# Optimization experiments

Measured on AMD Instinct MI355X. Metric: run time of the kernel, lower is better.

The kernel has to match this reference:

```python
import jax, jax.numpy as jnp
import numpy as np

B, C, H, W = 2, 256, 64, 64
NH, HD, K = 4, 64, 16  # num_head, head_channel, n_clusters
N = H * W
SCALE = HD ** 0.5


def _lin(x, Wm, b):
    return x @ Wm + b


def _mlp(x, W1, b1, W2, b2):
    h = _lin(x, W1, b1)
    h = jnp.where(h > 0, h, 0.01 * h)  # LeakyReLU(0.01)
    return _lin(h, W2, b2)  # dropout p=0.0 -> identity


def setup_inputs() -> dict:
    key = jax.random.key(0)
    ks = jax.random.split(key, 20)
    s = 1.0 / np.sqrt(C)
    s2 = 1.0 / np.sqrt(2 * C)
    inp = {
        "q_img": jax.random.normal(ks[0], (B, C, H, W), jnp.float32),
        "k_img_map": jax.random.normal(ks[1], (B, C, H, W), jnp.float32),
        "v_img_map": jax.random.normal(ks[2], (B, C, H, W), jnp.float32),
        "labels": jax.random.randint(ks[3], (B, H, W), 0, K),
        "pixel_coefficients": jax.random.uniform(ks[4], (B, N, N), jnp.float32),
        "Wq": jax.random.uniform(ks[5], (C, C), jnp.float32, -s, s),
        "bq": jnp.zeros((C,), jnp.float32),
        "Wk": jax.random.uniform(ks[6], (C, C), jnp.float32, -s, s),
        "bk": jnp.zeros((C,), jnp.float32),
        "Wv": jax.random.uniform(ks[7], (C, C), jnp.float32, -s, s),
        "bv": jnp.zeros((C,), jnp.float32),
        "W11": jax.random.uniform(ks[8], (C, 2 * C), jnp.float32, -s, s),
        "b11": jnp.zeros((2 * C,), jnp.float32),
        "W12": jax.random.uniform(ks[9], (2 * C, C), jnp.float32, -s2, s2),
        "b12": jnp.zeros((C,), jnp.float32),
        "W21": jax.random.uniform(ks[10], (C, 2 * C), jnp.float32, -s, s),
        "b21": jnp.zeros((2 * C,), jnp.float32),
        "W22": jax.random.uniform(ks[11], (2 * C, C), jnp.float32, -s2, s2),
        "b22": jnp.zeros((C,), jnp.float32),
    }
    return inp


def reference(q_img, k_img_map, v_img_map, labels, pixel_coefficients,
              Wq, bq, Wk, bk, Wv, bv, W11, b11, W12, b12, W21, b21, W22, b22):
    # [B,C,H,W] -> [B,N,C]
    q = _lin(q_img.transpose(0, 2, 3, 1).reshape(B, N, C), Wq, bq)
    k = _lin(k_img_map.transpose(0, 2, 3, 1).reshape(B, N, C), Wk, bk)
    v = _lin(v_img_map.transpose(0, 2, 3, 1).reshape(B, N, C), Wv, bv)

    lab = labels.reshape(B, N)
    onehot = (lab[:, :, None] == jnp.arange(K)[None, None, :]).astype(jnp.float32)  # [B,N,K]
    num_k = jnp.einsum('bnk,bnc->bkc', onehot, k)
    den_k = onehot.sum(axis=1)[:, :, None] + 1e-6
    centers_k = num_k / den_k  # [B,K,C]

    qm = q.reshape(B, N, NH, HD).transpose(0, 2, 1, 3)  # [B,h,N,d]
    km = k.reshape(B, N, NH, HD).transpose(0, 2, 1, 3)
    vm = v.reshape(B, N, NH, HD).transpose(0, 2, 1, 3)
    cm = centers_k.reshape(B, K, NH, HD).transpose(0, 2, 1, 3)  # [B,h,K,d]

    attn_intra = jnp.einsum('bhnd,bhmd->bhnm', qm, km)          # [B,h,N,N]
    attn_centers = jnp.einsum('bhnd,bhkd->bhnk', qm, cm)        # [B,h,N,K]

    same = (lab[:, :, None] == lab[:, None, :])[:, None]        # [B,1,N,N]
    idx = jnp.broadcast_to(lab[:, None, None, :], (B, NH, N, N))
    attn_inter = jnp.take_along_axis(attn_centers, idx, axis=-1) * pixel_coefficients[:, None]

    scores = jnp.where(same, attn_intra, attn_inter) / SCALE
    attn = jax.nn.softmax(scores, axis=-1)
    out = jnp.einsum('bhnm,bhmd->bhnd', attn, vm).transpose(0, 2, 1, 3).reshape(B, N, C)

    rs1 = v + _mlp(out, W11, b11, W12, b12)        # [B,N,C] (v_spatial residual)
    rs2 = rs1 + _mlp(rs1, W21, b21, W22, b22)
    return rs2.reshape(B, H, W, C).transpose(0, 3, 1, 2)  # [B,C,H,W]
```

## Files before the change

### kernel.cpp

```cpp
#include <hip/hip_runtime.h>
#include <stdint.h>

#define Bv 2
#define Cv 256
#define Nv 4096
#define NHv 4
#define HDv 64
#define Kv 16


typedef __attribute__((ext_vector_type(8))) short bf16x8;
typedef __attribute__((ext_vector_type(4))) float f32x4;

__device__ __forceinline__ float bf2f(unsigned short u) {
  union { unsigned int i; float f; } x; x.i = ((unsigned int)u) << 16; return x.f;
}
__device__ __forceinline__ unsigned short f2bf(float f) {
  union { float f; unsigned int i; } x; x.f = f;
  unsigned int r = x.i + 0x7FFF + ((x.i >> 16) & 1);
  return (unsigned short)(r >> 16);
}
__device__ __forceinline__ unsigned int cvt_pk_bf16(float lo, float hi) {
  unsigned int r;
  asm("v_cvt_pk_bf16_f32 %0, %1, %2" : "=v"(r) : "v"(lo), "v"(hi));
  return r;
}
__device__ __forceinline__ float exp2_raw(float x) {
  float r;
  asm("v_exp_f32 %0, %1" : "=v"(r) : "v"(x));
  return r;
}
__device__ __forceinline__ float bperm_f(int idx_bytes, float v) {
  return __int_as_float(__builtin_amdgcn_ds_bpermute(idx_bytes, __float_as_int(v)));
}

__global__ __launch_bounds__(256) void imgt_k(
    const float* __restrict__ qi, const float* __restrict__ ki,
    const float* __restrict__ vi, unsigned short* __restrict__ dst)
{
  const int z = blockIdx.z;
  const float* src = (z < 2 ? qi : (z < 4 ? ki : vi)) + (long long)(z & 1) * Cv * Nv;
  unsigned short* out = dst + (long long)z * Nv * Cv;
  __shared__ float t[32][33];
  const int x = threadIdx.x, y = threadIdx.y;
  const int n0 = blockIdx.x * 32, c0 = blockIdx.y * 32;
  for (int i = y; i < 32; i += 8)
    t[i][x] = src[(long long)(c0 + i) * Nv + n0 + x];
  __syncthreads();
  for (int i = y; i < 32; i += 8)
    out[(long long)(n0 + i) * Cv + c0 + x] = f2bf(t[x][i]);
}

struct WP { const float* p[7]; };

__global__ __launch_bounds__(256) void wt_k(WP wp, unsigned short* __restrict__ dst)
{
  const int z = blockIdx.z;
  const int KD[7] = {256, 256, 256, 256, 512, 256, 512};
  const int ND[7] = {256, 256, 256, 512, 256, 512, 256};
  const long long OFF[7] = {0, 65536, 131072, 196608, 327680, 458752, 589824};
  const int Kw = KD[z], Nw = ND[z];
  const int nb = blockIdx.x * 32, kb2 = blockIdx.y * 32;
  if (nb >= Nw || kb2 >= Kw) return;
  __shared__ float t[32][33];
  const int x = threadIdx.x, y = threadIdx.y;
  const float* src = wp.p[z];
  for (int i = y; i < 32; i += 8)
    t[i][x] = src[(long long)(kb2 + i) * Nw + nb + x];
  __syncthreads();
  for (int i = y; i < 32; i += 8)
    dst[OFF[z] + (long long)(nb + i) * Kw + kb2 + x] = f2bf(t[x][i]);
}

__global__ __launch_bounds__(256) void proj64_k(
    const unsigned short* __restrict__ imgT, const unsigned short* __restrict__ wt,
    const float* __restrict__ bq, const float* __restrict__ bk, const float* __restrict__ bv,
    unsigned short* __restrict__ qbf, unsigned short* __restrict__ kbf,
    float* __restrict__ vpp, unsigned short* __restrict__ vtb)
{
  __shared__ __align__(16) unsigned short As[64][72];
  __shared__ __align__(16) unsigned short Bs[64][72];
  const int tid = threadIdx.x;
  const int w = tid >> 6, lane = tid & 63;
  const int lr = lane & 15, quad = lane >> 4;
  const int m0 = blockIdx.x * 64, n0 = blockIdx.y * 64;
  const int z = blockIdx.z, zz = z >> 1, bb = z & 1;
  const int wm = (w >> 1) * 32, wn = (w & 1) * 32;
  const int sr = tid >> 2, sh = (tid & 3) * 16;
  const long long NvCv = (long long)Nv * Cv;

  const float* bias = zz == 0 ? bq : (zz == 1 ? bk : bv);
  const unsigned short* Ab0 = imgT + (long long)z * NvCv + (long long)(m0 + sr) * Cv + sh;
  const unsigned short* Bb0 = wt + (long long)zz * 65536 + (long long)(n0 + sr) * Cv + sh;

  f32x4 acc[2][2];
#pragma unroll
  for (int i = 0; i < 2; ++i)
#pragma unroll
    for (int j = 0; j < 2; ++j) acc[i][j] = (f32x4){0.f, 0.f, 0.f, 0.f};

  uint4 rA0 = *(const uint4*)Ab0, rA1 = *(const uint4*)(Ab0 + 8);
  uint4 rB0 = *(const uint4*)Bb0, rB1 = *(const uint4*)(Bb0 + 8);

  for (int k0 = 0; k0 < Cv; k0 += 64) {
    *(uint4*)&As[sr][sh] = rA0; *(uint4*)&As[sr][sh + 8] = rA1;
    *(uint4*)&Bs[sr][sh] = rB0; *(uint4*)&Bs[sr][sh + 8] = rB1;
    __syncthreads();
    if (k0 + 64 < Cv) {
      rA0 = *(const uint4*)(Ab0 + k0 + 64); rA1 = *(const uint4*)(Ab0 + k0 + 72);
      rB0 = *(const uint4*)(Bb0 + k0 + 64); rB1 = *(const uint4*)(Bb0 + k0 + 72);
    }
#pragma unroll
    for (int ks = 0; ks < 2; ++ks) {
      bf16x8 af[2], bfr[2];
#pragma unroll
      for (int i = 0; i < 2; ++i)
        af[i] = *(const bf16x8*)&As[wm + i * 16 + lr][ks * 32 + quad * 8];
#pragma unroll
      for (int j = 0; j < 2; ++j)
        bfr[j] = *(const bf16x8*)&Bs[wn + j * 16 + lr][ks * 32 + quad * 8];
#pragma unroll
      for (int i = 0; i < 2; ++i)
#pragma unroll
        for (int j = 0; j < 2; ++j)
          acc[i][j] = __builtin_amdgcn_mfma_f32_16x16x32_bf16(af[i], bfr[j], acc[i][j], 0, 0, 0);
    }
    __syncthreads();
  }

#pragma unroll
  for (int j = 0; j < 2; ++j) {
    const int col = n0 + wn + j * 16 + lr;
    const float bvv = bias[col];
#pragma unroll
    for (int i = 0; i < 2; ++i) {
      const int mb = m0 + wm + i * 16 + quad * 4;
      float r[4];
#pragma unroll
      for (int reg = 0; reg < 4; ++reg) r[reg] = acc[i][j][reg] + bvv;
      const long long ob = (long long)bb * NvCv;
      if (zz == 0) {
#pragma unroll
        for (int reg = 0; reg < 4; ++reg)
          qbf[ob + (long long)(mb + reg) * Cv + col] = f2bf(r[reg] * 0.18033688f);
      } else if (zz == 1) {
#pragma unroll
        for (int reg = 0; reg < 4; ++reg)
          kbf[ob + (long long)(mb + reg) * Cv + col] = f2bf(r[reg]);
      } else {
#pragma unroll
        for (int reg = 0; reg < 4; ++reg)
          vpp[ob + (long long)(mb + reg) * Cv + col] = r[reg];
        uint2 pk;
        pk.x = cvt_pk_bf16(r[0], r[1]);
        pk.y = cvt_pk_bf16(r[2], r[3]);
        *(uint2*)&vtb[ob + (long long)col * Nv + mb] = pk;
      }
    }
  }
}

template<bool ABF16, int ACT, int RES, int OM>
__global__ __launch_bounds__(256) void mm64_k(
    const void* __restrict__ A, const unsigned short* __restrict__ Bt,
    const float* __restrict__ bias, const float* __restrict__ Res,
    float* __restrict__ outF, unsigned short* __restrict__ outB,
    int M, int Nn, int Kd)
{
  __shared__ __align__(16) unsigned short As[64][72];
  __shared__ __align__(16) unsigned short Bs[64][72];
  const int tid = threadIdx.x;
  const int w = tid >> 6, lane = tid & 63;
  const int lr = lane & 15, quad = lane >> 4;
  const int m0 = blockIdx.x * 64, n0 = blockIdx.y * 64;
  const int wm = (w >> 1) * 32, wn = (w & 1) * 32;
  const int sr = tid >> 2, sh = (tid & 3) * 16;

  f32x4 acc[2][2];
#pragma unroll
  for (int i = 0; i < 2; ++i)
#pragma unroll
    for (int j = 0; j < 2; ++j) acc[i][j] = (f32x4){0.f, 0.f, 0.f, 0.f};

  const long long abase = (long long)(m0 + sr) * Kd + sh;
  const unsigned short* Bb = Bt + (long long)(n0 + sr) * Kd + sh;

  uint4 rA0, rA1, rB0, rB1;
  float4 fA[4];
  if (ABF16) {
    const unsigned short* Ab = (const unsigned short*)A + abase;
    rA0 = *(const uint4*)Ab; rA1 = *(const uint4*)(Ab + 8);
  } else {
    const float* Af = (const float*)A + abase;
    fA[0] = *(const float4*)Af;      fA[1] = *(const float4*)(Af + 4);
    fA[2] = *(const float4*)(Af + 8); fA[3] = *(const float4*)(Af + 12);
  }
  rB0 = *(const uint4*)Bb; rB1 = *(const uint4*)(Bb + 8);

  for (int k0 = 0; k0 < Kd; k0 += 64) {
    if (ABF16) {
      *(uint4*)&As[sr][sh] = rA0; *(uint4*)&As[sr][sh + 8] = rA1;
    } else {
#pragma unroll
      for (int t = 0; t < 2; ++t) {
        uint4 pk;
        pk.x = cvt_pk_bf16(fA[t * 2].x, fA[t * 2].y);
        pk.y = cvt_pk_bf16(fA[t * 2].z, fA[t * 2].w);
        pk.z = cvt_pk_bf16(fA[t * 2 + 1].x, fA[t * 2 + 1].y);
        pk.w = cvt_pk_bf16(fA[t * 2 + 1].z, fA[t * 2 + 1].w);
        *(uint4*)&As[sr][sh + t * 8] = pk;
      }
    }
    *(uint4*)&Bs[sr][sh] = rB0; *(uint4*)&Bs[sr][sh + 8] = rB1;
    __syncthreads();
    if (k0 + 64 < Kd) {
      if (ABF16) {
        const unsigned short* Ab = (const unsigned short*)A + abase + k0 + 64;
        rA0 = *(const uint4*)Ab; rA1 = *(const uint4*)(Ab + 8);
      } else {
        const float* Af = (const float*)A + abase + k0 + 64;
        fA[0] = *(const float4*)Af;      fA[1] = *(const float4*)(Af + 4);
        fA[2] = *(const float4*)(Af + 8); fA[3] = *(const float4*)(Af + 12);
      }
      rB0 = *(const uint4*)(Bb + k0 + 64); rB1 = *(const uint4*)(Bb + k0 + 72);
    }
#pragma unroll
    for (int ks = 0; ks < 2; ++ks) {
      bf16x8 af[2], bfr[2];
#pragma unroll
      for (int i = 0; i < 2; ++i)
        af[i] = *(const bf16x8*)&As[wm + i * 16 + lr][ks * 32 + quad * 8];
#pragma unroll
      for (int j = 0; j < 2; ++j)
        bfr[j] = *(const bf16x8*)&Bs[wn + j * 16 + lr][ks * 32 + quad * 8];
#pragma unroll
      for (int i = 0; i < 2; ++i)
#pragma unroll
        for (int j = 0; j < 2; ++j)
          acc[i][j] = __builtin_amdgcn_mfma_f32_16x16x32_bf16(af[i], bfr[j], acc[i][j], 0, 0, 0);
    }
    __syncthreads();
  }

#pragma unroll
  for (int j = 0; j < 2; ++j) {
    const int col = n0 + wn + j * 16 + lr;
    const float bv = bias[col];
#pragma unroll
    for (int i = 0; i < 2; ++i) {
      const int mb = m0 + wm + i * 16 + quad * 4;
      float r[4];
#pragma unroll
      for (int reg = 0; reg < 4; ++reg) {
        float v = acc[i][j][reg] + bv;
        if (ACT) v = v > 0.f ? v : 0.01f * v;
        if (RES) v += Res[(long long)(mb + reg) * Nn + col];
        r[reg] = v;
      }
      if (OM == 0) {
#pragma unroll
        for (int reg = 0; reg < 4; ++reg)
          outF[(long long)(mb + reg) * Nn + col] = r[reg];
      } else if (OM == 1) {
#pragma unroll
        for (int reg = 0; reg < 4; ++reg)
          outB[(long long)(mb + reg) * Nn + col] = f2bf(r[reg]);
      } else if (OM == 2) {
#pragma unroll
        for (int reg = 0; reg < 4; ++reg) {
          outF[(long long)(mb + reg) * Nn + col] = r[reg];
          outB[(long long)(mb + reg) * Nn + col] = f2bf(r[reg]);
        }
      } else {
        const float4 st = {r[0], r[1], r[2], r[3]};
        *(float4*)&outF[((long long)((mb >> 12) * Cv + col)) * Nv + (mb & 4095)] = st;
      }
    }
  }
}

__global__ __launch_bounds__(256) void zero_k(float* p, int n)
{
  const int i = blockIdx.x * 256 + threadIdx.x;
  if (i < n) p[i] = 0.f;
}

__global__ __launch_bounds__(256) void center_accum(
    const unsigned short* __restrict__ kb, const int* __restrict__ labels,
    float* __restrict__ cent, float* __restrict__ cnts)
{
  __shared__ int lab_s[512];
  const int bx = blockIdx.x;
  const int chunk = bx & 7;
  const int kk = (bx >> 3) & 15;
  const int b = bx >> 7;
  const int c = threadIdx.x;
  const int nbase = chunk * 512;
  for (int i = threadIdx.x; i < 512; i += 256) lab_s[i] = labels[b * Nv + nbase + i];
  __syncthreads();
  float acc = 0.f;
  int cnt = 0;
#pragma unroll 4
  for (int i = 0; i < 512; ++i) {
    if (lab_s[i] == kk) {
      acc += bf2f(kb[(long long)(b * Nv + nbase + i) * Cv + c]);
      ++cnt;
    }
  }
  atomicAdd(&cent[(b * Kv + kk) * Cv + c], acc);
  if (c == 0) atomicAdd(&cnts[b * Kv + kk], (float)cnt);
}

__global__ __launch_bounds__(256) void center_norm(float* cent, const float* cnts)
{
  const int i = blockIdx.x * 256 + threadIdx.x;
  cent[i] = cent[i] / (cnts[i >> 8] + 1e-6f);
}

union PSCS {
  unsigned short p[4][16][68];
  float c[16][68];
};

__global__ __launch_bounds__(256) void attn_k(
    const unsigned short* __restrict__ qb, const unsigned short* __restrict__ kb,
    const unsigned short* __restrict__ vtb, const float* __restrict__ cent,
    const int* __restrict__ labels, const float* __restrict__ pc,
    float* __restrict__ opart, float* __restrict__ lpart)
{
  __shared__ __align__(16) unsigned short q_s[64][72];
  __shared__ __align__(16) unsigned short k_s[64][72];
  __shared__ __align__(16) unsigned short vt_s[64][72];
  __shared__ __align__(16) PSCS u_s;
  __shared__ float ac_s[64][17];

  const int tid = threadIdx.x;
  const int lane = tid & 63, w = tid >> 6;
  const int lr = lane & 15, quad = lane >> 4;
  const int bx = blockIdx.x;
  const int qt = bx & 63, h = (bx >> 6) & 3, b = (bx >> 8) & 1;
  const int part = bx >> 9;
  const int n0 = qt * 64;
  const int mbase = part * 2048;
  const int sr2 = tid >> 2, so2 = (tid & 3) * 16;
  const int row_l = w * 16 + quad * 4;
  const long long pcb = (long long)b * Nv * Nv;

  {
    const unsigned short* src = qb + ((long long)(b * Nv + n0 + sr2)) * Cv + h * HDv + so2;
    *(uint4*)&q_s[sr2][so2] = *(const uint4*)src;
    *(uint4*)&q_s[sr2][so2 + 8] = *(const uint4*)(src + 8);
  }
  for (int idx = tid; idx < Kv * HDv; idx += 256)
    u_s.c[idx >> 6][idx & 63] = cent[((long long)(b * Kv + (idx >> 6))) * Cv + h * HDv + (idx & 63)];

  uint4 ka0, ka1, va0, va1;
  float pc1[4][4];
  int labm1[4], labq[4];
  {
    const long long ks = ((long long)(b * Nv + mbase + sr2)) * Cv + h * HDv + so2;
    ka0 = *(const uint4*)(kb + ks); ka1 = *(const uint4*)(kb + ks + 8);
    const long long vs = ((long long)(b * Cv + h * HDv + sr2)) * Nv + mbase + so2;
    va0 = *(const uint4*)(vtb + vs); va1 = *(const uint4*)(vtb + vs + 8);
  }
#pragma unroll
  for (int sub = 0; sub < 4; ++sub) {
    labm1[sub] = labels[b * Nv + mbase + sub * 16 + lr];
#pragma unroll
    for (int reg = 0; reg < 4; ++reg)
      pc1[sub][reg] = pc[pcb + (long long)(n0 + row_l + reg) * Nv + mbase + sub * 16 + lr];
  }
#pragma unroll
  for (int reg = 0; reg < 4; ++reg) labq[reg] = labels[b * Nv + n0 + row_l + reg];

  __syncthreads();
  for (int idx = tid; idx < 64 * Kv; idx += 256) {
    const int r = idx >> 4, kk = idx & 15;
    float s = 0.f;
#pragma unroll
    for (int d = 0; d < HDv; ++d) s += bf2f(q_s[r][d]) * u_s.c[kk][d];
    ac_s[r][kk] = s;
  }
  const bf16x8 qa0 = *(const bf16x8*)&q_s[w * 16 + lr][quad * 8];
  const bf16x8 qa1 = *(const bf16x8*)&q_s[w * 16 + lr][32 + quad * 8];
  __syncthreads();

  float acv[4];
#pragma unroll
  for (int reg = 0; reg < 4; ++reg) acv[reg] = ac_s[w * 16 + quad * 4 + reg][lr];

  float acg[4][4];
#pragma unroll
  for (int sub = 0; sub < 4; ++sub) {
    const int bidx = (quad << 6) + (labm1[sub] << 2);
#pragma unroll
    for (int reg = 0; reg < 4; ++reg)
      acg[sub][reg] = bperm_f(bidx, acv[reg]);
  }

  *(uint4*)&k_s[sr2][so2] = ka0; *(uint4*)&k_s[sr2][so2 + 8] = ka1;
  *(uint4*)&vt_s[sr2][so2] = va0; *(uint4*)&vt_s[sr2][so2 + 8] = va1;
  __syncthreads();

  f32x4 oacc[4];
#pragma unroll
  for (int s2 = 0; s2 < 4; ++s2) oacc[s2] = (f32x4){0.f, 0.f, 0.f, 0.f};
  float lrow[4] = {0.f, 0.f, 0.f, 0.f};

  for (int t = 0; t < 32; ++t) {
    const int m0 = mbase + t * 64;
    const bool has = (t < 31);

    if (has) {
      const long long ks = ((long long)(b * Nv + m0 + 64 + sr2)) * Cv + h * HDv + so2;
      ka0 = *(const uint4*)(kb + ks); ka1 = *(const uint4*)(kb + ks + 8);
      const long long vs = ((long long)(b * Cv + h * HDv + sr2)) * Nv + m0 + 64 + so2;
      va0 = *(const uint4*)(vtb + vs); va1 = *(const uint4*)(vtb + vs + 8);
    }

    f32x4 sacc[4];
    __builtin_amdgcn_s_setprio(1);
#pragma unroll
    for (int sub = 0; sub < 4; ++sub) {
      const bf16x8 kb0 = *(const bf16x8*)&k_s[sub * 16 + lr][quad * 8];
      const bf16x8 kb1 = *(const bf16x8*)&k_s[sub * 16 + lr][32 + quad * 8];
      f32x4 s = (f32x4){0.f, 0.f, 0.f, 0.f};
      s = __builtin_amdgcn_mfma_f32_16x16x32_bf16(qa0, kb0, s, 0, 0, 0);
      s = __builtin_amdgcn_mfma_f32_16x16x32_bf16(qa1, kb1, s, 0, 0, 0);
      sacc[sub] = s;
    }
    __builtin_amdgcn_s_setprio(0);

#pragma unroll
    for (int sub = 0; sub < 4; ++sub) {
      float p4[4];
#pragma unroll
      for (int reg = 0; reg < 4; ++reg) {
        const float s = (labm1[sub] == labq[reg]) ? sacc[sub][reg]
                                                  : acg[sub][reg] * pc1[sub][reg];
        const float p = exp2_raw(s);
        lrow[reg] += p;
        p4[reg] = p;
      }
      const unsigned int pk01 = cvt_pk_bf16(p4[0], p4[1]);
      const unsigned int pk23 = cvt_pk_bf16(p4[2], p4[3]);
      unsigned short* pp = &u_s.p[w][quad * 4][sub * 16 + lr];
      pp[0]   = (unsigned short)pk01;
      pp[68]  = (unsigned short)(pk01 >> 16);
      pp[136] = (unsigned short)pk23;
      pp[204] = (unsigned short)(pk23 >> 16);
    }

    if (has) {
#pragma unroll
      for (int sub = 0; sub < 4; ++sub) {
        labm1[sub] = labels[b * Nv + m0 + 64 + sub * 16 + lr];
#pragma unroll
        for (int reg = 0; reg < 4; ++reg)
          pc1[sub][reg] = pc[pcb + (long long)(n0 + row_l + reg) * Nv + m0 + 64 + sub * 16 + lr];
      }
    }

    const bf16x8 pa0 = *(const bf16x8*)&u_s.p[w][lr][quad * 8];
    const bf16x8 pa1 = *(const bf16x8*)&u_s.p[w][lr][32 + quad * 8];
    __builtin_amdgcn_s_setprio(1);
#pragma unroll
    for (int sub = 0; sub < 4; ++sub) {
      const bf16x8 vb0 = *(const bf16x8*)&vt_s[sub * 16 + lr][quad * 8];
      const bf16x8 vb1 = *(const bf16x8*)&vt_s[sub * 16 + lr][32 + quad * 8];
      oacc[sub] = __builtin_amdgcn_mfma_f32_16x16x32_bf16(pa0, vb0, oacc[sub], 0, 0, 0);
      oacc[sub] = __builtin_amdgcn_mfma_f32_16x16x32_bf16(pa1, vb1, oacc[sub], 0, 0, 0);
    }
    __builtin_amdgcn_s_setprio(0);

    if (has) {
#pragma unroll
      for (int sub = 0; sub < 4; ++sub) {
        const int bidx = (quad << 6) + (labm1[sub] << 2);
#pragma unroll
        for (int reg = 0; reg < 4; ++reg)
          acg[sub][reg] = bperm_f(bidx, acv[reg]);
      }
    }

    __syncthreads();
    if (has) {
      *(uint4*)&k_s[sr2][so2] = ka0; *(uint4*)&k_s[sr2][so2 + 8] = ka1;
      *(uint4*)&vt_s[sr2][so2] = va0; *(uint4*)&vt_s[sr2][so2 + 8] = va1;
    }
    __syncthreads();
  }

#pragma unroll
  for (int reg = 0; reg < 4; ++reg) {
    float l = lrow[reg];
    l += __shfl_xor(l, 1); l += __shfl_xor(l, 2);
    l += __shfl_xor(l, 4); l += __shfl_xor(l, 8);
    const int row = n0 + row_l + reg;
    const long long obase = (long long)part * 2097152 + ((long long)(b * Nv + row)) * Cv + h * HDv;
#pragma unroll
    for (int sub = 0; sub < 4; ++sub)
      opart[obase + sub * 16 + lr] = oacc[sub][reg];
    if (lr == 0)
      lpart[part * 32768 + (b * 4 + h) * 4096 + row] = l;
  }
}

__global__ __launch_bounds__(256) void combine_k(
    const float* __restrict__ op, const float* __restrict__ lp,
    unsigned short* __restrict__ aob)
{
  const long long i4 = ((long long)blockIdx.x * 256 + threadIdx.x) * 4;
  const int c = (int)(i4 & 255), n = (int)((i4 >> 8) & 4095), b = (int)(i4 >> 20);
  const int h = c >> 6;
  const float l = lp[(b * 4 + h) * 4096 + n] + lp[32768 + (b * 4 + h) * 4096 + n];
  const float inv = 1.f / l;
  const float4 a = *(const float4*)&op[i4];
  const float4 d = *(const float4*)&op[2097152 + i4];
  uint2 pk;
  pk.x = cvt_pk_bf16((a.x + d.x) * inv, (a.y + d.y) * inv);
  pk.y = cvt_pk_bf16((a.z + d.z) * inv, (a.w + d.w) * inv);
  *(uint2*)&aob[i4] = pk;
}

extern "C" void kernel_launch(void* const* d_in, const int* in_sizes, int n_in,
                              void* d_out, int out_size, void* d_ws, size_t ws_size,
                              hipStream_t stream)
{
  const float* q_img = (const float*)d_in[0];
  const float* k_img = (const float*)d_in[1];
  const float* v_img = (const float*)d_in[2];
  const int* labels  = (const int*)d_in[3];
  const float* pc    = (const float*)d_in[4];
  const float* Wq  = (const float*)d_in[5];  const float* bq  = (const float*)d_in[6];
  const float* Wk  = (const float*)d_in[7];  const float* bk  = (const float*)d_in[8];
  const float* Wv  = (const float*)d_in[9];  const float* bv  = (const float*)d_in[10];
  const float* W11 = (const float*)d_in[11]; const float* b11 = (const float*)d_in[12];
  const float* W12 = (const float*)d_in[13]; const float* b12 = (const float*)d_in[14];
  const float* W21 = (const float*)d_in[15]; const float* b21 = (const float*)d_in[16];
  const float* W22 = (const float*)d_in[17]; const float* b22 = (const float*)d_in[18];
  float* outp = (float*)d_out;

  const long long SZ = (long long)Bv * Nv * Cv;
  float* ws    = (float*)d_ws;
  float* vpp   = ws;
  float* rs1   = vpp + SZ;
  float* opart = rs1 + SZ;
  float* lpart = opart + 2 * SZ;
  float* cent  = lpart + 65536;
  float* cnts  = cent + Bv * Kv * Cv;
  unsigned short* wt   = (unsigned short*)(cnts + Bv * Kv);
  unsigned short* qbf  = wt + 720896;
  unsigned short* kbf  = qbf + SZ;
  unsigned short* vtb  = kbf + SZ;
  unsigned short* aob  = vtb + SZ;
  unsigned short* h1b  = aob + SZ;
  unsigned short* imgT = aob;

  imgt_k<<<dim3(Nv / 32, Cv / 32, 6), dim3(32, 8), 0, stream>>>(q_img, k_img, v_img, imgT);
  WP wp = {{Wq, Wk, Wv, W11, W12, W21, W22}};
  wt_k<<<dim3(16, 16, 7), dim3(32, 8), 0, stream>>>(wp, wt);

  proj64_k<<<dim3(64, 4, 6), 256, 0, stream>>>(imgT, wt, bq, bk, bv, qbf, kbf, vpp, vtb);

  zero_k<<<dim3(33), 256, 0, stream>>>(cent, Bv * Kv * Cv + Bv * Kv);
  center_accum<<<dim3(Bv * Kv * 8), 256, 0, stream>>>(kbf, labels, cent, cnts);
  center_norm<<<dim3(Bv * Kv * Cv / 256), 256, 0, stream>>>(cent, cnts);

  attn_k<<<dim3(1024), 256, 0, stream>>>(qbf, kbf, vtb, cent, labels, pc, opart, lpart);
  combine_k<<<dim3(2048), 256, 0, stream>>>(opart, lpart, aob);

  mm64_k<true, 1, 0, 1><<<dim3(128, 8), 256, 0, stream>>>(
      aob, wt + 196608, b11, nullptr, nullptr, h1b, 2 * Nv, 2 * Cv, Cv);
  mm64_k<true, 0, 1, 2><<<dim3(128, 4), 256, 0, stream>>>(
      h1b, wt + 327680, b12, vpp, rs1, aob, 2 * Nv, Cv, 2 * Cv);

  mm64_k<true, 1, 0, 1><<<dim3(128, 8), 256, 0, stream>>>(
      aob, wt + 458752, b21, nullptr, nullptr, h1b, 2 * Nv, 2 * Cv, Cv);
  mm64_k<true, 0, 1, 4><<<dim3(128, 4), 256, 0, stream>>>(
      h1b, wt + 589824, b22, rs1, outp, nullptr, 2 * Nv, Cv, 2 * Cv);
}
```

Baseline: 403.6 us.

## Fuse zeroing and center normalization, double-buffer GEMM LDS, cut attention LDS usage

Folds the zeroing of the center accumulators into the weight-transpose launch and moves the center normalization into the attention kernel, removing two small launches. The MLP GEMM now double-buffers its shared-memory tiles so one barrier per k-step can be dropped. The attention kernel reuses the q and k tiles for its P and center scratch and reads gathered center scores from LDS instead of lane permutes. It prefetches pixel coefficients two tiles ahead and declares occupancy 4. Memory pressure and kernel count go down, but the new code relies on subtle barrier ordering when it reuses buffers.

```diff
diff --git a/kernel.cpp b/kernel.cpp
--- a/kernel.cpp
+++ b/kernel.cpp
@@ -29,9 +29,6 @@
   float r;
   asm("v_exp_f32 %0, %1" : "=v"(r) : "v"(x));
   return r;
-}
-__device__ __forceinline__ float bperm_f(int idx_bytes, float v) {
-  return __int_as_float(__builtin_amdgcn_ds_bpermute(idx_bytes, __float_as_int(v)));
 }
 
 __global__ __launch_bounds__(256) void imgt_k(
@@ -53,9 +50,15 @@
 
 struct WP { const float* p[7]; };
 
-__global__ __launch_bounds__(256) void wt_k(WP wp, unsigned short* __restrict__ dst)
+__global__ __launch_bounds__(256) void wt_k(WP wp, unsigned short* __restrict__ dst,
+                                            float* __restrict__ zp, int zn)
 {
   const int z = blockIdx.z;
+  if (z == 7) {
+    const int idx = (blockIdx.y * 16 + blockIdx.x) * 256 + threadIdx.y * 32 + threadIdx.x;
+    if (idx < zn) zp[idx] = 0.f;
+    return;
+  }
   const int KD[7] = {256, 256, 256, 256, 512, 256, 512};
   const int ND[7] = {256, 256, 256, 512, 256, 512, 256};
   const long long OFF[7] = {0, 65536, 131072, 196608, 327680, 458752, 589824};
@@ -167,8 +170,8 @@
     float* __restrict__ outF, unsigned short* __restrict__ outB,
     int M, int Nn, int Kd)
 {
-  __shared__ __align__(16) unsigned short As[64][72];
-  __shared__ __align__(16) unsigned short Bs[64][72];
+  __shared__ __align__(16) unsigned short As[2][64][72];
+  __shared__ __align__(16) unsigned short Bs[2][64][72];
   const int tid = threadIdx.x;
   const int w = tid >> 6, lane = tid & 63;
   const int lr = lane & 15, quad = lane >> 4;
@@ -197,9 +200,10 @@
   }
   rB0 = *(const uint4*)Bb; rB1 = *(const uint4*)(Bb + 8);
 
+  int buf = 0;
   for (int k0 = 0; k0 < Kd; k0 += 64) {
     if (ABF16) {
-      *(uint4*)&As[sr][sh] = rA0; *(uint4*)&As[sr][sh + 8] = rA1;
+      *(uint4*)&As[buf][sr][sh] = rA0; *(uint4*)&As[buf][sr][sh + 8] = rA1;
     } else {
 #pragma unroll
       for (int t = 0; t < 2; ++t) {
@@ -208,10 +212,10 @@
         pk.y = cvt_pk_bf16(fA[t * 2].z, fA[t * 2].w);
         pk.z = cvt_pk_bf16(fA[t * 2 + 1].x, fA[t * 2 + 1].y);
         pk.w = cvt_pk_bf16(fA[t * 2 + 1].z, fA[t * 2 + 1].w);
-        *(uint4*)&As[sr][sh + t * 8] = pk;
+        *(uint4*)&As[buf][sr][sh + t * 8] = pk;
       }
     }
-    *(uint4*)&Bs[sr][sh] = rB0; *(uint4*)&Bs[sr][sh + 8] = rB1;
+    *(uint4*)&Bs[buf][sr][sh] = rB0; *(uint4*)&Bs[buf][sr][sh + 8] = rB1;
     __syncthreads();
     if (k0 + 64 < Kd) {
       if (ABF16) {
@@ -229,17 +233,17 @@
       bf16x8 af[2], bfr[2];
 #pragma unroll
       for (int i = 0; i < 2; ++i)
-        af[i] = *(const bf16x8*)&As[wm + i * 16 + lr][ks * 32 + quad * 8];
+        af[i] = *(const bf16x8*)&As[buf][wm + i * 16 + lr][ks * 32 + quad * 8];
 #pragma unroll
       for (int j = 0; j < 2; ++j)
-        bfr[j] = *(const bf16x8*)&Bs[wn + j * 16 + lr][ks * 32 + quad * 8];
+        bfr[j] = *(const bf16x8*)&Bs[buf][wn + j * 16 + lr][ks * 32 + quad * 8];
 #pragma unroll
       for (int i = 0; i < 2; ++i)
 #pragma unroll
         for (int j = 0; j < 2; ++j)
           acc[i][j] = __builtin_amdgcn_mfma_f32_16x16x32_bf16(af[i], bfr[j], acc[i][j], 0, 0, 0);
     }
-    __syncthreads();
+    buf ^= 1;
   }
 
 #pragma unroll
@@ -277,12 +281,6 @@
       }
     }
   }
-}
-
-__global__ __launch_bounds__(256) void zero_k(float* p, int n)
-{
-  const int i = blockIdx.x * 256 + threadIdx.x;
-  if (i < n) p[i] = 0.f;
 }
 
 __global__ __launch_bounds__(256) void center_accum(
@@ -311,27 +309,15 @@
   if (c == 0) atomicAdd(&cnts[b * Kv + kk], (float)cnt);
 }
 
-__global__ __launch_bounds__(256) void center_norm(float* cent, const float* cnts)
-{
-  const int i = blockIdx.x * 256 + threadIdx.x;
-  cent[i] = cent[i] / (cnts[i >> 8] + 1e-6f);
-}
-
-union PSCS {
-  unsigned short p[4][16][68];
-  float c[16][68];
-};
-
-__global__ __launch_bounds__(256) void attn_k(
+__global__ __launch_bounds__(256, 4) void attn_k(
     const unsigned short* __restrict__ qb, const unsigned short* __restrict__ kb,
     const unsigned short* __restrict__ vtb, const float* __restrict__ cent,
-    const int* __restrict__ labels, const float* __restrict__ pc,
-    float* __restrict__ opart, float* __restrict__ lpart)
+    const float* __restrict__ cnts, const int* __restrict__ labels,
+    const float* __restrict__ pc, float* __restrict__ opart, float* __restrict__ lpart)
 {
   __shared__ __align__(16) unsigned short q_s[64][72];
   __shared__ __align__(16) unsigned short k_s[64][72];
   __shared__ __align__(16) unsigned short vt_s[64][72];
-  __shared__ __align__(16) PSCS u_s;
   __shared__ float ac_s[64][17];
 
   const int tid = threadIdx.x;
@@ -351,11 +337,15 @@
     *(uint4*)&q_s[sr2][so2] = *(const uint4*)src;
     *(uint4*)&q_s[sr2][so2 + 8] = *(const uint4*)(src + 8);
   }
-  for (int idx = tid; idx < Kv * HDv; idx += 256)
-    u_s.c[idx >> 6][idx & 63] = cent[((long long)(b * Kv + (idx >> 6))) * Cv + h * HDv + (idx & 63)];
+  float* c_s = (float*)&k_s[0][0];
+  for (int idx = tid; idx < Kv * HDv; idx += 256) {
+    const int kk = idx >> 6, d = idx & 63;
+    c_s[kk * 68 + d] = cent[((long long)(b * Kv + kk)) * Cv + h * HDv + d]
+                       / (cnts[b * Kv + kk] + 1e-6f);
+  }
 
   uint4 ka0, ka1, va0, va1;
-  float pc1[4][4];
+  float pcA[4][4], pcB[4][4];
   int labm1[4], labq[4];
   {
     const long long ks = ((long long)(b * Nv + mbase + sr2)) * Cv + h * HDv + so2;
@@ -367,8 +357,10 @@
   for (int sub = 0; sub < 4; ++sub) {
     labm1[sub] = labels[b * Nv + mbase + sub * 16 + lr];
 #pragma unroll
-    for (int reg = 0; reg < 4; ++reg)
-      pc1[sub][reg] = pc[pcb + (long long)(n0 + row_l + reg) * Nv + mbase + sub * 16 + lr];
+    for (int reg = 0; reg < 4; ++reg) {
+      pcA[sub][reg] = pc[pcb + (long long)(n0 + row_l + reg) * Nv + mbase + sub * 16 + lr];
+      pcB[sub][reg] = pc[pcb + (long long)(n0 + row_l + reg) * Nv + mbase + 64 + sub * 16 + lr];
+    }
   }
 #pragma unroll
   for (int reg = 0; reg < 4; ++reg) labq[reg] = labels[b * Nv + n0 + row_l + reg];
@@ -378,25 +370,19 @@
     const int r = idx >> 4, kk = idx & 15;
     float s = 0.f;
 #pragma unroll
-    for (int d = 0; d < HDv; ++d) s += bf2f(q_s[r][d]) * u_s.c[kk][d];
+    for (int d = 0; d < HDv; ++d) s += bf2f(q_s[r][d]) * c_s[kk * 68 + d];
     ac_s[r][kk] = s;
   }
   const bf16x8 qa0 = *(const bf16x8*)&q_s[w * 16 + lr][quad * 8];
   const bf16x8 qa1 = *(const bf16x8*)&q_s[w * 16 + lr][32 + quad * 8];
   __syncthreads();
 
-  float acv[4];
-#pragma unroll
-  for (int reg = 0; reg < 4; ++reg) acv[reg] = ac_s[w * 16 + quad * 4 + reg][lr];
-
   float acg[4][4];
 #pragma unroll
-  for (int sub = 0; sub < 4; ++sub) {
-    const int bidx = (quad << 6) + (labm1[sub] << 2);
+  for (int sub = 0; sub < 4; ++sub)
 #pragma unroll
     for (int reg = 0; reg < 4; ++reg)
-      acg[sub][reg] = bperm_f(bidx, acv[reg]);
-  }
+      acg[sub][reg] = ac_s[row_l + reg][labm1[sub]];
 
   *(uint4*)&k_s[sr2][so2] = ka0; *(uint4*)&k_s[sr2][so2 + 8] = ka1;
   *(uint4*)&vt_s[sr2][so2] = va0; *(uint4*)&vt_s[sr2][so2 + 8] = va1;
@@ -407,89 +393,95 @@
   for (int s2 = 0; s2 < 4; ++s2) oacc[s2] = (f32x4){0.f, 0.f, 0.f, 0.f};
   float lrow[4] = {0.f, 0.f, 0.f, 0.f};
 
-  for (int t = 0; t < 32; ++t) {
-    const int m0 = mbase + t * 64;
-    const bool has = (t < 31);
-
-    if (has) {
-      const long long ks = ((long long)(b * Nv + m0 + 64 + sr2)) * Cv + h * HDv + so2;
-      ka0 = *(const uint4*)(kb + ks); ka1 = *(const uint4*)(kb + ks + 8);
-      const long long vs = ((long long)(b * Cv + h * HDv + sr2)) * Nv + m0 + 64 + so2;
-      va0 = *(const uint4*)(vtb + vs); va1 = *(const uint4*)(vtb + vs + 8);
-    }
-
-    f32x4 sacc[4];
-    __builtin_amdgcn_s_setprio(1);
-#pragma unroll
-    for (int sub = 0; sub < 4; ++sub) {
-      const bf16x8 kb0 = *(const bf16x8*)&k_s[sub * 16 + lr][quad * 8];
-      const bf16x8 kb1 = *(const bf16x8*)&k_s[sub * 16 + lr][32 + quad * 8];
-      f32x4 s = (f32x4){0.f, 0.f, 0.f, 0.f};
-      s = __builtin_amdgcn_mfma_f32_16x16x32_bf16(qa0, kb0, s, 0, 0, 0);
-      s = __builtin_amdgcn_mfma_f32_16x16x32_bf16(qa1, kb1, s, 0, 0, 0);
-      sacc[sub] = s;
-    }
-    __builtin_amdgcn_s_setprio(0);
-
-#pragma unroll
-    for (int sub = 0; sub < 4; ++sub) {
-      float p4[4];
-#pragma unroll
-      for (int reg = 0; reg < 4; ++reg) {
-        const float s = (labm1[sub] == labq[reg]) ? sacc[sub][reg]
-                                                  : acg[sub][reg] * pc1[sub][reg];
-        const float p = exp2_raw(s);
-        lrow[reg] += p;
-        p4[reg] = p;
-      }
-      const unsigned int pk01 = cvt_pk_bf16(p4[0], p4[1]);
-      const unsigned int pk23 = cvt_pk_bf16(p4[2], p4[3]);
-      unsigned short* pp = &u_s.p[w][quad * 4][sub * 16 + lr];
-      pp[0]   = (unsigned short)pk01;
-      pp[68]  = (unsigned short)(pk01 >> 16);
-      pp[136] = (unsigned short)pk23;
-      pp[204] = (unsigned short)(pk23 >> 16);
-    }
-
-    if (has) {
-#pragma unroll
-      for (int sub = 0; sub < 4; ++sub) {
-        labm1[sub] = labels[b * Nv + m0 + 64 + sub * 16 + lr];
-#pragma unroll
-        for (int reg = 0; reg < 4; ++reg)
-          pc1[sub][reg] = pc[pcb + (long long)(n0 + row_l + reg) * Nv + m0 + 64 + sub * 16 + lr];
-      }
-    }
-
-    const bf16x8 pa0 = *(const bf16x8*)&u_s.p[w][lr][quad * 8];
-    const bf16x8 pa1 = *(const bf16x8*)&u_s.p[w][lr][32 + quad * 8];
-    __builtin_amdgcn_s_setprio(1);
-#pragma unroll
-    for (int sub = 0; sub < 4; ++sub) {
-      const bf16x8 vb0 = *(const bf16x8*)&vt_s[sub * 16 + lr][quad * 8];
-      const bf16x8 vb1 = *(const bf16x8*)&vt_s[sub * 16 + lr][32 + quad * 8];
-      oacc[sub] = __builtin_amdgcn_mfma_f32_16x16x32_bf16(pa0, vb0, oacc[sub], 0, 0, 0);
-      oacc[sub] = __builtin_amdgcn_mfma_f32_16x16x32_bf16(pa1, vb1, oacc[sub], 0, 0, 0);
-    }
-    __builtin_amdgcn_s_setprio(0);
-
-    if (has) {
-#pragma unroll
-      for (int sub = 0; sub < 4; ++sub) {
-        const int bidx = (quad << 6) + (labm1[sub] << 2);
-#pragma unroll
-        for (int reg = 0; reg < 4; ++reg)
-          acg[sub][reg] = bperm_f(bidx, acv[reg]);
-      }
-    }
-
-    __syncthreads();
-    if (has) {
-      *(uint4*)&k_s[sr2][so2] = ka0; *(uint4*)&k_s[sr2][so2 + 8] = ka1;
-      *(uint4*)&vt_s[sr2][so2] = va0; *(uint4*)&vt_s[sr2][so2 + 8] = va1;
-    }
-    __syncthreads();
-  }
+#define ATTN_TILE(PCREG)                                                        \
+  {                                                                             \
+    const int m0 = mbase + t * 64;                                              \
+    const bool has1 = (t < 31);                                                 \
+    const bool has2 = (t < 30);                                                 \
+    if (has1) {                                                                 \
+      const long long ks = ((long long)(b * Nv + m0 + 64 + sr2)) * Cv + h * HDv + so2; \
+      ka0 = *(const uint4*)(kb + ks); ka1 = *(const uint4*)(kb + ks + 8);       \
+      const long long vs = ((long long)(b * Cv + h * HDv + sr2)) * Nv + m0 + 64 + so2; \
+      va0 = *(const uint4*)(vtb + vs); va1 = *(const uint4*)(vtb + vs + 8);     \
+    }                                                                           \
+    f32x4 sacc[4];                                                              \
+    __builtin_amdgcn_s_setprio(1);                                              \
+    _Pragma("unroll")                                                           \
+    for (int sub = 0; sub < 4; ++sub) {                                         \
+      const bf16x8 kf0 = *(const bf16x8*)&k_s[sub * 16 + lr][quad * 8];         \
+      const bf16x8 kf1 = *(const bf16x8*)&k_s[sub * 16 + lr][32 + quad * 8];    \
+      f32x4 s = (f32x4){0.f, 0.f, 0.f, 0.f};                                    \
+      s = __builtin_amdgcn_mfma_f32_16x16x32_bf16(qa0, kf0, s, 0, 0, 0);        \
+      s = __builtin_amdgcn_mfma_f32_16x16x32_bf16(qa1, kf1, s, 0, 0, 0);        \
+      sacc[sub] = s;                                                            \
+    }                                                                           \
+    __builtin_amdgcn_s_setprio(0);                                              \
+    _Pragma("unroll")                                                           \
+    for (int sub = 0; sub < 4; ++sub) {                                         \
+      float p4[4];                                                              \
+      _Pragma("unroll")                                                         \
+      for (int reg = 0; reg < 4; ++reg) {                                       \
+        const float s = (labm1[sub] == labq[reg]) ? sacc[sub][reg]              \
+                                                  : acg[sub][reg] * PCREG[sub][reg]; \
+        const float p = exp2_raw(s);                                            \
+        lrow[reg] += p;                                                         \
+        p4[reg] = p;                                                            \
+      }                                                                         \
+      const unsigned int pk01 = cvt_pk_bf16(p4[0], p4[1]);                      \
+      const unsigned int pk23 = cvt_pk_bf16(p4[2], p4[3]);                      \
+      unsigned short* pp = &q_s[w * 16 + quad * 4][sub * 16 + lr];              \
+      pp[0]   = (unsigned short)pk01;                                           \
+      pp[72]  = (unsigned short)(pk01 >> 16);                                   \
+      pp[144] = (unsigned short)pk23;                                           \
+      pp[216] = (unsigned short)(pk23 >> 16);                                   \
+    }                                                                           \
+    if (has1) {                                                                 \
+      _Pragma("unroll")                                                         \
+      for (int sub = 0; sub < 4; ++sub)                                         \
+        labm1[sub] = labels[b * Nv + m0 + 64 + sub * 16 + lr];                  \
+    }                                                                           \
+    if (has2) {                                                                 \
+      _Pragma("unroll")                                                         \
+      for (int sub = 0; sub < 4; ++sub) {                                       \
+        _Pragma("unroll")                                                       \
+        for (int reg = 0; reg < 4; ++reg)                                       \
+          PCREG[sub][reg] = pc[pcb + (long long)(n0 + row_l + reg) * Nv + m0 + 128 + sub * 16 + lr]; \
+      }                                                                         \
+    }                                                                           \
+    const bf16x8 pa0 = *(const bf16x8*)&q_s[w * 16 + lr][quad * 8];             \
+    const bf16x8 pa1 = *(const bf16x8*)&q_s[w * 16 + lr][32 + quad * 8];        \
+    __builtin_amdgcn_s_setprio(1);                                              \
+    _Pragma("unroll")                                                           \
+    for (int sub = 0; sub < 4; ++sub) {                                         \
+      const bf16x8 vb0 = *(const bf16x8*)&vt_s[sub * 16 + lr][quad * 8];        \
+      const bf16x8 vb1 = *(const bf16x8*)&vt_s[sub * 16 + lr][32 + quad * 8];   \
+      oacc[sub] = __builtin_amdgcn_mfma_f32_16x16x32_bf16(pa0, vb0, oacc[sub], 0, 0, 0); \
+      oacc[sub] = __builtin_amdgcn_mfma_f32_16x16x32_bf16(pa1, vb1, oacc[sub], 0, 0, 0); \
+    }                                                                           \
+    __builtin_amdgcn_s_setprio(0);                                              \
+    if (has1) {                                                                 \
+      _Pragma("unroll")                                                         \
+      for (int sub = 0; sub < 4; ++sub) {                                       \
+        _Pragma("unroll")                                                       \
+        for (int reg = 0; reg < 4; ++reg)                                       \
+          acg[sub][reg] = ac_s[row_l + reg][labm1[sub]];                        \
+      }                                                                         \
+    }                                                                           \
+    __syncthreads();                                                            \
+    if (has1) {                                                                 \
+      *(uint4*)&k_s[sr2][so2] = ka0; *(uint4*)&k_s[sr2][so2 + 8] = ka1;         \
+      *(uint4*)&vt_s[sr2][so2] = va0; *(uint4*)&vt_s[sr2][so2 + 8] = va1;       \
+    }                                                                           \
+    __syncthreads();                                                            \
+    ++t;                                                                        \
+  }
+
+  int t = 0;
+  for (int it = 0; it < 16; ++it) {
+    ATTN_TILE(pcA)
+    ATTN_TILE(pcB)
+  }
+#undef ATTN_TILE
 
 #pragma unroll
   for (int reg = 0; reg < 4; ++reg) {
@@ -559,15 +551,13 @@
 
   imgt_k<<<dim3(Nv / 32, Cv / 32, 6), dim3(32, 8), 0, stream>>>(q_img, k_img, v_img, imgT);
   WP wp = {{Wq, Wk, Wv, W11, W12, W21, W22}};
-  wt_k<<<dim3(16, 16, 7), dim3(32, 8), 0, stream>>>(wp, wt);
+  wt_k<<<dim3(16, 16, 8), dim3(32, 8), 0, stream>>>(wp, wt, cent, Bv * Kv * Cv + Bv * Kv);
 
   proj64_k<<<dim3(64, 4, 6), 256, 0, stream>>>(imgT, wt, bq, bk, bv, qbf, kbf, vpp, vtb);
 
-  zero_k<<<dim3(33), 256, 0, stream>>>(cent, Bv * Kv * Cv + Bv * Kv);
   center_accum<<<dim3(Bv * Kv * 8), 256, 0, stream>>>(kbf, labels, cent, cnts);
-  center_norm<<<dim3(Bv * Kv * Cv / 256), 256, 0, stream>>>(cent, cnts);
-
-  attn_k<<<dim3(1024), 256, 0, stream>>>(qbf, kbf, vtb, cent, labels, pc, opart, lpart);
+
+  attn_k<<<dim3(1024), 256, 0, stream>>>(qbf, kbf, vtb, cent, cnts, labels, pc, opart, lpart);
   combine_k<<<dim3(2048), 256, 0, stream>>>(opart, lpart, aob);
 
   mm64_k<true, 1, 0, 1><<<dim3(128, 8), 256, 0, stream>>>(
```

Result: slower. 728.9 us (+80.6%).
